# Optimization experiments

Measured on AMD Instinct MI355X. Metric: run time of the kernel, lower is better.

Reference implementation:

```python
import jax, jax.numpy as jnp
import numpy as np

B, SQ, SK, D, H, HD = 2, 2048, 2048, 1024, 16, 64


def setup_inputs() -> dict:
    key = jax.random.key(0)
    ks = jax.random.split(key, 10)
    s = 1.0 / np.sqrt(D)  # keep activations well-scaled
    return {
        "x": jax.random.normal(ks[0], (B, SQ, D), jnp.float32),
        "encoder_output": jax.random.normal(ks[1], (B, SK, D), jnp.float32),
        "Wq": jax.random.normal(ks[2], (H, D, HD), jnp.float32) * s,
        "bq": jax.random.normal(ks[3], (H, HD), jnp.float32) * 0.01,
        "Wk": jax.random.normal(ks[4], (H, D, HD), jnp.float32) * s,
        "bk": jax.random.normal(ks[5], (H, HD), jnp.float32) * 0.01,
        "Wv": jax.random.normal(ks[6], (H, D, HD), jnp.float32) * s,
        "bv": jax.random.normal(ks[7], (H, HD), jnp.float32) * 0.01,
        "Wo": jax.random.normal(ks[8], (D, D), jnp.float32) * s,
        "bo": jax.random.normal(ks[9], (D,), jnp.float32) * 0.01,
    }


def reference(x, encoder_output, Wq, bq, Wk, bk, Wv, bv, Wo, bo):
    # Batched per-head projections (equivalent to the per-head nn.Linear loop).
    q = jnp.einsum('bsd,hde->bhse', x, Wq) + bq[None, :, None, :]              # [B,H,SQ,HD]
    k = jnp.einsum('bsd,hde->bhse', encoder_output, Wk) + bk[None, :, None, :]  # [B,H,SK,HD]
    v = jnp.einsum('bsd,hde->bhse', encoder_output, Wv) + bv[None, :, None, :]  # [B,H,SK,HD]
    scale = 1.0 / jnp.sqrt(jnp.asarray(HD, q.dtype))
    scores = jnp.einsum('bhqe,bhke->bhqk', q, k) * scale                        # [B,H,SQ,SK]
    attn = jax.nn.softmax(scores, axis=-1)
    out = jnp.einsum('bhqk,bhke->bhqe', attn, v)                                # [B,H,SQ,HD]
    # concat heads along feature dim (head order matches torch.cat order)
    out = out.transpose(0, 2, 1, 3).reshape(out.shape[0], out.shape[2], -1)     # [B,SQ,D]
    # final linear; dropout is identity in eval mode
    return out @ Wo + bo
```

## Files before the change

kernel.cpp:

```cpp
#include <hip/hip_runtime.h>


typedef unsigned short u16;
typedef __bf16 bf16x8 __attribute__((ext_vector_type(8)));
typedef float f32x4 __attribute__((ext_vector_type(4)));
typedef float f32x16 __attribute__((ext_vector_type(16)));
typedef unsigned u32x2 __attribute__((ext_vector_type(2)));

#define B_ 2
#define SQ_ 2048
#define SK_ 2048
#define D_ 1024
#define H_ 16
#define HD_ 64

__device__ __forceinline__ u16 f2bf(float f) {
  union { float f; unsigned u; } c; c.f = f;
  unsigned u = c.u;
  return (u16)((u + 0x7fffu + ((u >> 16) & 1u)) >> 16);
}
__device__ __forceinline__ float bf2f(u16 h) {
  union { unsigned u; float f; } c; c.u = ((unsigned)h) << 16;
  return c.f;
}
__device__ __forceinline__ unsigned pack_bf16(float lo, float hi) {
  union { __bf16 h[2]; unsigned u; } c;
  c.h[0] = (__bf16)lo;
  c.h[1] = (__bf16)hi;
  return c.u;
}

#define GLOAD_LDS16(gp, lp)                                                  \
  __builtin_amdgcn_global_load_lds(                                          \
      (const __attribute__((address_space(1))) void*)(gp),                   \
      (__attribute__((address_space(3))) void*)(lp), 16, 0, 0)

__global__ __launch_bounds__(256) void prep_fused(const float* __restrict__ x,
                                                  const float* __restrict__ enc,
                                                  const float* __restrict__ Wq,
                                                  const float* __restrict__ Wk,
                                                  const float* __restrict__ Wv,
                                                  const float* __restrict__ Wo,
                                                  u16* __restrict__ xb,
                                                  u16* __restrict__ eb,
                                                  u16* __restrict__ WqT,
                                                  u16* __restrict__ WoT) {
  __shared__ float tile[64][65];
  const int id = blockIdx.x;
  const int tid = threadIdx.x;

  if (id < 8192) {
    const float* in = (id >= 4096) ? enc : x;
    u16* out = (id >= 4096) ? eb : xb;
    int i = (id & 4095) * 256 + tid;
    float4 v = ((const float4*)in)[i];
    uint2 p;
    p.x = (unsigned)f2bf(v.x) | ((unsigned)f2bf(v.y) << 16);
    p.y = (unsigned)f2bf(v.z) | ((unsigned)f2bf(v.w) << 16);
    ((uint2*)out)[i] = p;
    return;
  }

  if (id < 8960) {
    const int f = id - 8192;
    const int z48 = f >> 4, y = f & 15;
    const int mat = z48 >> 4, head = z48 & 15;
    const float* W = (mat == 0) ? Wq : (mat == 1 ? Wk : Wv);
    const float* ib = W + (long)head * 65536;
    u16* ob = WqT + ((long)mat << 20) + (long)head * 65536;
    const int r0 = y << 6;
#pragma unroll
    for (int i = 0; i < 16; ++i) {
      int idx = tid + (i << 8);
      int r = idx >> 6, c = idx & 63;
      tile[r][c] = ib[(long)(r0 + r) * 64 + c];
    }
    __syncthreads();
#pragma unroll
    for (int i = 0; i < 16; ++i) {
      int idx = tid + (i << 8);
      int cc = idx >> 6, rr = idx & 63;
      ob[(long)cc * 1024 + (r0 + rr)] = f2bf(tile[rr][cc]);
    }
    return;
  }

  {
    const int g = id - 8960;
    const int c0 = (g & 15) << 6, r0 = (g >> 4) << 6;
#pragma unroll
    for (int i = 0; i < 16; ++i) {
      int idx = tid + (i << 8);
      int r = idx >> 6, c = idx & 63;
      tile[r][c] = Wo[(long)(r0 + r) * 1024 + (c0 + c)];
    }
    __syncthreads();
#pragma unroll
    for (int i = 0; i < 16; ++i) {
      int idx = tid + (i << 8);
      int cc = idx >> 6, rr = idx & 63;
      WoT[(long)(c0 + cc) * 1024 + (r0 + rr)] = f2bf(tile[rr][cc]);
    }
  }
}

__global__ __launch_bounds__(256) void gemm_qkv(const u16* __restrict__ xb,
                                                const u16* __restrict__ eb,
                                                const u16* __restrict__ Wt3,
                                                const float* __restrict__ bq,
                                                const float* __restrict__ bk,
                                                const float* __restrict__ bv,
                                                u16* __restrict__ qws,
                                                u16* __restrict__ kws,
                                                u16* __restrict__ vT) {
  constexpr int M = 2048, N = 1024, K = 1024;
  __shared__ __align__(16) u16 As[128 * 64];
  __shared__ __align__(16) u16 Bs[128 * 64];
  const int tid = threadIdx.x;
  const int lane = tid & 63;
  const int wid = tid >> 6;
  const int l16 = lane & 15, quad = lane >> 4;
  const int wm = wid >> 1, wn = wid & 1;
  const int bn0g = blockIdx.x << 7;
  const int seg = bn0g >> 10;
  const int bn0 = bn0g & (N - 1);
  const int bm0 = blockIdx.y << 7;
  const u16* A = (seg == 0) ? xb : eb;
  const u16* Wt = Wt3 + ((long)seg << 20);
  const float* bias = (seg == 0) ? bq : (seg == 1 ? bk : bv);
  const long abase = (long)blockIdx.z * M * K;

  f32x4 acc[4][4];
#pragma unroll
  for (int i = 0; i < 4; ++i)
#pragma unroll
    for (int j = 0; j < 4; ++j) acc[i][j] = f32x4{0.f, 0.f, 0.f, 0.f};

  const int r0 = tid >> 3;
  const int c0s = ((tid & 7) ^ (r0 & 7)) << 3;
  const u16* agp = A + abase + (long)(bm0 + r0) * K + c0s;
  const u16* bgp = Wt + (long)(bn0 + r0) * K + c0s;
  u16* alp = As + tid * 8;
  u16* blp = Bs + tid * 8;

  for (int k0 = 0; k0 < K; k0 += 64) {
#pragma unroll
    for (int i = 0; i < 4; ++i) {
      GLOAD_LDS16(agp + k0 + (long)(32 * i) * K, alp + i * 2048);
      GLOAD_LDS16(bgp + k0 + (long)(32 * i) * K, blp + i * 2048);
    }
    __syncthreads();
#pragma unroll
    for (int kk = 0; kk < 2; ++kk) {
      const int csw = ((quad + 4 * kk) ^ (l16 & 7)) << 3;
      bf16x8 af[4], bfr[4];
#pragma unroll
      for (int mi = 0; mi < 4; ++mi)
        af[mi] = *(const bf16x8*)(As + (wm * 64 + mi * 16 + l16) * 64 + csw);
#pragma unroll
      for (int ni = 0; ni < 4; ++ni)
        bfr[ni] = *(const bf16x8*)(Bs + (wn * 64 + ni * 16 + l16) * 64 + csw);
#pragma unroll
      for (int mi = 0; mi < 4; ++mi)
#pragma unroll
        for (int ni = 0; ni < 4; ++ni)
          acc[mi][ni] = __builtin_amdgcn_mfma_f32_16x16x32_bf16(af[mi], bfr[ni],
                                                                acc[mi][ni], 0, 0, 0);
    }
    __syncthreads();
  }

  float bv4[4];
#pragma unroll
  for (int ni = 0; ni < 4; ++ni) bv4[ni] = bias[bn0 + wn * 64 + ni * 16 + l16];

  if (seg == 2) {
    const long zb = (long)blockIdx.z * N * M;
#pragma unroll
    for (int mi = 0; mi < 4; ++mi)
#pragma unroll
      for (int ni = 0; ni < 4; ++ni) {
        int colg = bn0 + wn * 64 + ni * 16 + l16;
        int rowg = bm0 + wm * 64 + mi * 16 + (quad << 2);
        ushort4 pk = make_ushort4(f2bf(acc[mi][ni][0] + bv4[ni]),
                                  f2bf(acc[mi][ni][1] + bv4[ni]),
                                  f2bf(acc[mi][ni][2] + bv4[ni]),
                                  f2bf(acc[mi][ni][3] + bv4[ni]));
        *(ushort4*)(vT + zb + (long)colg * M + rowg) = pk;
      }
  } else {
    u16* outp = seg ? kws : qws;
    const long cbase = (long)blockIdx.z * M * N;
#pragma unroll
    for (int mi = 0; mi < 4; ++mi)
#pragma unroll
      for (int ni = 0; ni < 4; ++ni)
#pragma unroll
        for (int r = 0; r < 4; ++r) {
          int row = bm0 + wm * 64 + mi * 16 + (quad << 2) + r;
          int col = bn0 + wn * 64 + ni * 16 + l16;
          outp[cbase + (long)row * N + col] = f2bf(acc[mi][ni][r] + bv4[ni]);
        }
  }
}

__global__ __launch_bounds__(256) void gemm_final(const u16* __restrict__ A,
                                                  const u16* __restrict__ Wt,
                                                  const float* __restrict__ bias,
                                                  float* __restrict__ C) {
  constexpr int M = 2048, N = 1024, K = 1024;
  __shared__ __align__(16) u16 As[64 * 64];
  __shared__ __align__(16) u16 Bs[128 * 64];
  const int tid = threadIdx.x;
  const int lane = tid & 63;
  const int wid = tid >> 6;
  const int l16 = lane & 15, quad = lane >> 4;
  const int bn0 = blockIdx.x << 7, bm0 = blockIdx.y << 6;

  f32x4 acc[4][2];
#pragma unroll
  for (int i = 0; i < 4; ++i)
#pragma unroll
    for (int j = 0; j < 2; ++j) acc[i][j] = f32x4{0.f, 0.f, 0.f, 0.f};

  const int r0 = tid >> 3;
  const int c0s = ((tid & 7) ^ (r0 & 7)) << 3;
  const long abase = (long)blockIdx.z * M * K;
  const u16* agp = A + abase + (long)(bm0 + r0) * K + c0s;
  const u16* bgp = Wt + (long)(bn0 + r0) * K + c0s;
  u16* alp = As + tid * 8;
  u16* blp = Bs + tid * 8;

  for (int k0 = 0; k0 < K; k0 += 64) {
#pragma unroll
    for (int i = 0; i < 2; ++i)
      GLOAD_LDS16(agp + k0 + (long)(32 * i) * K, alp + i * 2048);
#pragma unroll
    for (int i = 0; i < 4; ++i)
      GLOAD_LDS16(bgp + k0 + (long)(32 * i) * K, blp + i * 2048);
    __syncthreads();
#pragma unroll
    for (int kk = 0; kk < 2; ++kk) {
      const int csw = ((quad + 4 * kk) ^ (l16 & 7)) << 3;
      bf16x8 af[4], bfr[2];
#pragma unroll
      for (int mi = 0; mi < 4; ++mi)
        af[mi] = *(const bf16x8*)(As + (mi * 16 + l16) * 64 + csw);
#pragma unroll
      for (int ni = 0; ni < 2; ++ni)
        bfr[ni] = *(const bf16x8*)(Bs + (wid * 32 + ni * 16 + l16) * 64 + csw);
#pragma unroll
      for (int mi = 0; mi < 4; ++mi)
#pragma unroll
        for (int ni = 0; ni < 2; ++ni)
          acc[mi][ni] = __builtin_amdgcn_mfma_f32_16x16x32_bf16(af[mi], bfr[ni],
                                                                acc[mi][ni], 0, 0, 0);
    }
    __syncthreads();
  }

  float bv2[2];
#pragma unroll
  for (int ni = 0; ni < 2; ++ni) bv2[ni] = bias[bn0 + wid * 32 + ni * 16 + l16];
  const long cbase = (long)blockIdx.z * M * N;
#pragma unroll
  for (int mi = 0; mi < 4; ++mi)
#pragma unroll
    for (int ni = 0; ni < 2; ++ni)
#pragma unroll
      for (int r = 0; r < 4; ++r) {
        int row = bm0 + mi * 16 + (quad << 2) + r;
        int col = bn0 + wid * 32 + ni * 16 + l16;
        C[cbase + (long)row * N + col] = acc[mi][ni][r] + bv2[ni];
      }
}

#define ATTN_STAGE(kbase, vbase)                                              \
  do {                                                                        \
    GLOAD_LDS16(kp, (kbase) + st * 8);                                        \
    GLOAD_LDS16(kp + (long)32 * D_, (kbase) + 2048 + st * 8);                 \
    GLOAD_LDS16(vp, (vbase) + st * 8);                                        \
    GLOAD_LDS16(vp + (long)32 * SK_, (vbase) + 2048 + st * 8);                \
    kp += (long)64 * D_;                                                      \
    vp += 64;                                                                 \
  } while (0)

#define QK_BLOCK(Kb, sx0, sx1)                                                \
  do {                                                                        \
    {                                                                         \
      bf16x8 kf0 = *(const bf16x8*)((Kb) + ro0 + sw[0]);                      \
      bf16x8 kf1 = *(const bf16x8*)((Kb) + 2048 + ro0 + sw[0]);               \
      sx0 = __builtin_amdgcn_mfma_f32_32x32x16_bf16(kf0, qf[0], ZV, 0, 0, 0); \
      sx1 = __builtin_amdgcn_mfma_f32_32x32x16_bf16(kf1, qf[0], ZV, 0, 0, 0); \
    }                                                                         \
    _Pragma("unroll") for (int j = 1; j < 4; ++j) {                           \
      bf16x8 kf0 = *(const bf16x8*)((Kb) + ro0 + sw[j]);                      \
      bf16x8 kf1 = *(const bf16x8*)((Kb) + 2048 + ro0 + sw[j]);               \
      sx0 = __builtin_amdgcn_mfma_f32_32x32x16_bf16(kf0, qf[j], sx0, 0, 0, 0);\
      sx1 = __builtin_amdgcn_mfma_f32_32x32x16_bf16(kf1, qf[j], sx1, 0, 0, 0);\
    }                                                                         \
  } while (0)

#define EXPD(sx0, sx1)                                                        \
  do {                                                                        \
    _Pragma("unroll") for (int g = 0; g < 8; ++g) {                           \
      float a0 = __expf(sx0[2 * g]);                                          \
      float a1 = __expf(sx0[2 * g + 1]);                                      \
      float b0 = __expf(sx1[2 * g]);                                          \
      float b1 = __expf(sx1[2 * g + 1]);                                      \
      psA += a0 + a1;                                                         \
      psB += b0 + b1;                                                         \
      d0[g] = pack_bf16(a0, a1);                                              \
      d1[g] = pack_bf16(b0, b1);                                              \
    }                                                                         \
  } while (0)

#define PV_KS(Vb, dd, k1, ks)                                                 \
  do {                                                                        \
    u32x2 sA = __builtin_amdgcn_permlane32_swap(dd[4 * (k1)],                 \
                                                dd[4 * (k1) + 2], false,      \
                                                false);                       \
    u32x2 sB = __builtin_amdgcn_permlane32_swap(dd[4 * (k1) + 1],             \
                                                dd[4 * (k1) + 3], false,      \
                                                false);                       \
    union { unsigned u[4]; bf16x8 v; } pa;                                    \
    pa.u[0] = sA[0]; pa.u[1] = sB[0]; pa.u[2] = sA[1]; pa.u[3] = sB[1];       \
    bf16x8 v0 = *(const bf16x8*)((Vb) + ro0 + sw[ks]);                        \
    bf16x8 v1 = *(const bf16x8*)((Vb) + 2048 + ro0 + sw[ks]);                 \
    o0 = __builtin_amdgcn_mfma_f32_32x32x16_bf16(pa.v, v0, o0, 0, 0, 0);      \
    o1 = __builtin_amdgcn_mfma_f32_32x32x16_bf16(pa.v, v1, o1, 0, 0, 0);      \
  } while (0)

#define PV4(Vb)                                                               \
  do {                                                                        \
    PV_KS(Vb, d0, 0, 0);                                                      \
    PV_KS(Vb, d0, 1, 1);                                                      \
    PV_KS(Vb, d1, 0, 2);                                                      \
    PV_KS(Vb, d1, 1, 3);                                                      \
  } while (0)

__global__ __launch_bounds__(512) void attn_flash(const u16* __restrict__ q,
                                                  const u16* __restrict__ k,
                                                  const u16* __restrict__ vT,
                                                  u16* __restrict__ ctx) {
  __shared__ __align__(16) u16 SM[32768];

  const int tid = threadIdx.x;
  const int lane = tid & 63;
  const int wid = tid >> 6;
  const int half = wid >> 2;
  const int wq = wid & 3;
  const int l31 = lane & 31, h5 = lane >> 5;
  const int h = blockIdx.y, b = blockIdx.z;
  const int q0w = (blockIdx.x << 7) + (wq << 5);

  u16* Ksh = SM + half * 8192;
  u16* Vsh = SM + 16384 + half * 8192;

  bf16x8 qf[4];
  const u16* qp = q + ((long)(b * SQ_ + q0w + l31) * D_ + h * HD_ + 8 * h5);
#pragma unroll
  for (int j = 0; j < 4; ++j) {
    bf16x8 t = *(const bf16x8*)(qp + 16 * j);
#pragma unroll
    for (int e = 0; e < 8; ++e) t[e] = (__bf16)((float)t[e] * 0.125f);
    qf[j] = t;
  }

  const int st = tid & 255;
  const int srow = st >> 3;
  const int ssw = ((st & 7) ^ (srow & 7)) << 3;
  const u16* kp = k + ((long)(b * SK_ + (half << 10) + srow) * D_ + h * HD_ + ssw);
  const u16* vp = vT + ((long)(b * D_ + h * HD_ + srow) * SK_ + (half << 10) + ssw);

  const int ro0 = l31 << 6;
  int sw[4];
#pragma unroll
  for (int i = 0; i < 4; ++i) sw[i] = ((2 * i + h5) ^ (lane & 7)) << 3;

  f32x16 o0, o1, sA0, sA1;
  f32x16 ZV = {};
#pragma unroll
  for (int i = 0; i < 16; ++i) { o0[i] = 0.f; o1[i] = 0.f; }
  float psA = 0.f, psB = 0.f;
  unsigned d0[8], d1[8];

  ATTN_STAGE(Ksh, Vsh);

  for (int t = 0; t < 16; ++t) {
    const int cur = t & 1;
    __syncthreads();
    if (t < 15) ATTN_STAGE(Ksh + (cur ^ 1) * 4096, Vsh + (cur ^ 1) * 4096);
    QK_BLOCK(Ksh + cur * 4096, sA0, sA1);
    EXPD(sA0, sA1);
    PV4(Vsh + cur * 4096);
  }

  float ps = psA + psB;
  ps += __shfl_xor(ps, 32, 64);

  __syncthreads();
  float* cb = (float*)SM;
  const int wl = (wq << 6) | lane;
  if (half) {
#pragma unroll
    for (int r = 0; r < 16; ++r) {
      cb[r * 257 + wl] = o0[r];
      cb[(r + 16) * 257 + wl] = o1[r];
    }
    cb[8300 + wl] = ps;
  }
  __syncthreads();
  if (!half) {
#pragma unroll
    for (int r = 0; r < 16; ++r) {
      o0[r] += cb[r * 257 + wl];
      o1[r] += cb[(r + 16) * 257 + wl];
    }
    ps += cb[8300 + wl];
    float inv = 1.f / ps;
#pragma unroll
    for (int r = 0; r < 16; ++r) {
      const int crow = (r & 3) + 8 * (r >> 2) + 4 * h5;
      float dq = __shfl(inv, crow, 64);
      long base = (long)(b * SQ_ + q0w + crow) * D_ + h * HD_ + l31;
      ctx[base] = f2bf(o0[r] * dq);
      ctx[base + 32] = f2bf(o1[r] * dq);
    }
  }
}

extern "C" void kernel_launch(void* const* d_in, const int* in_sizes, int n_in,
                              void* d_out, int out_size, void* d_ws, size_t ws_size,
                              hipStream_t stream) {
  const float* x   = (const float*)d_in[0];
  const float* enc = (const float*)d_in[1];
  const float* Wq  = (const float*)d_in[2];
  const float* bq  = (const float*)d_in[3];
  const float* Wk  = (const float*)d_in[4];
  const float* bk  = (const float*)d_in[5];
  const float* Wv  = (const float*)d_in[6];
  const float* bv  = (const float*)d_in[7];
  const float* Wo  = (const float*)d_in[8];
  const float* bo  = (const float*)d_in[9];

  const long NE_X = (long)B_ * SQ_ * D_;
  const long NE_W = (long)D_ * D_;

  u16* outA = (u16*)d_out;
  u16* outB = outA + NE_X;
  u16* eb  = outB;
  u16* vTp = outA;

  u16* ws  = (u16*)d_ws;
  u16* WqT = ws;
  u16* WoT = WqT + 3 * NE_W;
  u16* qws = WoT + NE_W;
  u16* kws = qws + NE_X;
  u16* xb  = kws + NE_X;
  u16* ctx = xb;

  prep_fused<<<dim3(9216, 1, 1), 256, 0, stream>>>(x, enc, Wq, Wk, Wv, Wo,
                                                   xb, eb, WqT, WoT);

  gemm_qkv<<<dim3(24, 16, 2), 256, 0, stream>>>(xb, eb, WqT, bq, bk, bv,
                                                qws, kws, vTp);

  attn_flash<<<dim3(SQ_ / 128, H_, B_), 512, 0, stream>>>(qws, kws, vTp, ctx);

  gemm_final<<<dim3(8, 32, 2), 256, 0, stream>>>(ctx, WoT, bo, (float*)d_out);
}
```

Before: 210.3 us.

## Rewrite QKV GEMM with 256x256 tiles, double-buffered LDS and prioritized MFMA pipeline

The QKV projection GEMM moves from 128x128 tiles with 256 threads to 256x256 tiles with 512 threads (8 waves, each 128x64). It double-buffers the K slices in 128KB of LDS, issuing global-to-LDS loads for the next slice while the MFMAs for the current one run, with hand-placed barriers, waitcnts and setprio. This aims to hide global load latency and raise data reuse per tile. The cost is a grid of only 192 blocks with heavy LDS use (one block per CU), which may underfill the 256 CUs, plus fragile manual synchronization.

```diff
diff --git a/kernel.cpp b/kernel.cpp
--- a/kernel.cpp
+++ b/kernel.cpp
@@ -18,10 +18,6 @@
   union { float f; unsigned u; } c; c.f = f;
   unsigned u = c.u;
   return (u16)((u + 0x7fffu + ((u >> 16) & 1u)) >> 16);
-}
-__device__ __forceinline__ float bf2f(u16 h) {
-  union { unsigned u; float f; } c; c.u = ((unsigned)h) << 16;
-  return c.f;
 }
 __device__ __forceinline__ unsigned pack_bf16(float lo, float hi) {
   union { __bf16 h[2]; unsigned u; } c;
@@ -104,7 +100,55 @@
   }
 }
 
-__global__ __launch_bounds__(256) void gemm_qkv(const u16* __restrict__ xb,
+#define QBAR() asm volatile("s_barrier" ::: "memory")
+#define VMW4 asm volatile("s_waitcnt vmcnt(4)" ::: "memory")
+#define VMW0 asm volatile("s_waitcnt vmcnt(0)" ::: "memory")
+#define LGKM0 asm volatile("s_waitcnt lgkmcnt(0)" ::: "memory")
+#define PRIO1 __builtin_amdgcn_s_setprio(1)
+#define PRIO0 __builtin_amdgcn_s_setprio(0)
+
+#define ST_SLICE(gp, koff, dstu)                                              \
+  do {                                                                        \
+    GLOAD_LDS16((gp) + (koff), SMu + (dstu) + tid * 8);                       \
+    GLOAD_LDS16((gp) + (koff) + (long)128 * 1024, SMu + (dstu) + 4096 + tid * 8); \
+  } while (0)
+
+#define LDA4(dst, bufo, kko, mho)                                             \
+  _Pragma("unroll") for (int m2 = 0; m2 < 4; ++m2)                            \
+      dst[m2] = *(const bf16x8*)(SMu + (bufo) + (kko) + aob + (mho) + m2 * 512)
+
+#define LDB4(dst, bufo, kko)                                                  \
+  _Pragma("unroll") for (int n2 = 0; n2 < 4; ++n2)                            \
+      dst[n2] = *(const bf16x8*)(SMu + (bufo) + 16384 + (kko) + bob + n2 * 512)
+
+#define MM16(mh, av, bv_)                                                     \
+  _Pragma("unroll") for (int m2 = 0; m2 < 4; ++m2)                            \
+  _Pragma("unroll") for (int n2 = 0; n2 < 4; ++n2)                            \
+      acc[(mh) * 4 + m2][n2] = __builtin_amdgcn_mfma_f32_16x16x32_bf16(       \
+          av[m2], bv_[n2], acc[(mh) * 4 + m2][n2], 0, 0, 0)
+
+#define TILE_BODY(bo, so, kn)                                                 \
+  {                                                                           \
+    bf16x8 aF[4], aG[4], bF[4];                                               \
+                                      \
+    LDA4(aF, bo, 0, 0); LDB4(bF, bo, 0);                                      \
+    ST_SLICE(aS, (kn), (so) + 0);                                             \
+    QBAR(); LGKM0; PRIO1; MM16(0, aF, bF); PRIO0; QBAR();                     \
+                    \
+    LDA4(aG, bo, 0, 2048);                                                    \
+    ST_SLICE(bS, (kn), (so) + 16384);                                         \
+    QBAR(); LGKM0; PRIO1; MM16(1, aG, bF); PRIO0; VMW4; QBAR();               \
+                                      \
+    LDA4(aF, bo, 8192, 0); LDB4(bF, bo, 8192);                                \
+    ST_SLICE(aS, (kn) + 32, (so) + 8192);                                     \
+    QBAR(); LGKM0; PRIO1; MM16(0, aF, bF); PRIO0; QBAR();                     \
+                  \
+    LDA4(aG, bo, 8192, 2048);                                                 \
+    ST_SLICE(bS, (kn) + 32, (so) + 24576);                                    \
+    QBAR(); LGKM0; PRIO1; MM16(1, aG, bF); PRIO0; VMW4; QBAR();               \
+  }
+
+__global__ __launch_bounds__(512) void gemm_qkv(const u16* __restrict__ xb,
                                                 const u16* __restrict__ eb,
                                                 const u16* __restrict__ Wt3,
                                                 const float* __restrict__ bq,
@@ -114,60 +158,61 @@
                                                 u16* __restrict__ kws,
                                                 u16* __restrict__ vT) {
   constexpr int M = 2048, N = 1024, K = 1024;
-  __shared__ __align__(16) u16 As[128 * 64];
-  __shared__ __align__(16) u16 Bs[128 * 64];
+  __shared__ __align__(16) u16 SMu[65536];
+
   const int tid = threadIdx.x;
   const int lane = tid & 63;
   const int wid = tid >> 6;
+  const int wm = wid >> 2;
+  const int wn = wid & 3;
   const int l16 = lane & 15, quad = lane >> 4;
-  const int wm = wid >> 1, wn = wid & 1;
-  const int bn0g = blockIdx.x << 7;
+  const int qsw = (quad ^ ((l16 >> 1) & 3)) << 3;
+  const int aob = wm * 4096 + l16 * 32 + qsw;
+  const int bob = wn * 2048 + l16 * 32 + qsw;
+
+  const int bn0g = blockIdx.x << 8;
   const int seg = bn0g >> 10;
   const int bn0 = bn0g & (N - 1);
-  const int bm0 = blockIdx.y << 7;
+  const int bm0 = blockIdx.y << 8;
   const u16* A = (seg == 0) ? xb : eb;
   const u16* Wt = Wt3 + ((long)seg << 20);
   const float* bias = (seg == 0) ? bq : (seg == 1 ? bk : bv);
   const long abase = (long)blockIdx.z * M * K;
 
-  f32x4 acc[4][4];
-#pragma unroll
-  for (int i = 0; i < 4; ++i)
+  f32x4 acc[8][4];
+#pragma unroll
+  for (int i = 0; i < 8; ++i)
 #pragma unroll
     for (int j = 0; j < 4; ++j) acc[i][j] = f32x4{0.f, 0.f, 0.f, 0.f};
 
-  const int r0 = tid >> 3;
-  const int c0s = ((tid & 7) ^ (r0 & 7)) << 3;
-  const u16* agp = A + abase + (long)(bm0 + r0) * K + c0s;
-  const u16* bgp = Wt + (long)(bn0 + r0) * K + c0s;
-  u16* alp = As + tid * 8;
-  u16* blp = Bs + tid * 8;
-
-  for (int k0 = 0; k0 < K; k0 += 64) {
-#pragma unroll
-    for (int i = 0; i < 4; ++i) {
-      GLOAD_LDS16(agp + k0 + (long)(32 * i) * K, alp + i * 2048);
-      GLOAD_LDS16(bgp + k0 + (long)(32 * i) * K, blp + i * 2048);
-    }
-    __syncthreads();
-#pragma unroll
-    for (int kk = 0; kk < 2; ++kk) {
-      const int csw = ((quad + 4 * kk) ^ (l16 & 7)) << 3;
-      bf16x8 af[4], bfr[4];
-#pragma unroll
-      for (int mi = 0; mi < 4; ++mi)
-        af[mi] = *(const bf16x8*)(As + (wm * 64 + mi * 16 + l16) * 64 + csw);
-#pragma unroll
-      for (int ni = 0; ni < 4; ++ni)
-        bfr[ni] = *(const bf16x8*)(Bs + (wn * 64 + ni * 16 + l16) * 64 + csw);
-#pragma unroll
-      for (int mi = 0; mi < 4; ++mi)
-#pragma unroll
-        for (int ni = 0; ni < 4; ++ni)
-          acc[mi][ni] = __builtin_amdgcn_mfma_f32_16x16x32_bf16(af[mi], bfr[ni],
-                                                                acc[mi][ni], 0, 0, 0);
-    }
-    __syncthreads();
+  const int sr = tid >> 2;
+  const int sc2 = ((tid & 3) ^ ((sr >> 1) & 3)) << 3;
+  const u16* aS = A + abase + (long)(bm0 + sr) * K + sc2;
+  const u16* bS = Wt + (long)(bn0 + sr) * K + sc2;
+
+  ST_SLICE(aS, 0, 0);
+  ST_SLICE(bS, 0, 16384);
+  ST_SLICE(aS, 32, 8192);
+  ST_SLICE(bS, 32, 24576);
+  VMW4; QBAR();
+
+#pragma unroll 1
+  for (int tp = 0; tp < 7; ++tp) {
+    const int kb = tp * 128;
+    TILE_BODY(0, 32768, kb + 64);
+    TILE_BODY(32768, 0, kb + 128);
+  }
+  TILE_BODY(0, 32768, 960);
+  {
+    bf16x8 aF[4], aG[4], bF[4];
+    LDA4(aF, 32768, 0, 0); LDB4(bF, 32768, 0);
+    QBAR(); LGKM0; PRIO1; MM16(0, aF, bF); PRIO0; QBAR();
+    LDA4(aG, 32768, 0, 2048);
+    QBAR(); LGKM0; PRIO1; MM16(1, aG, bF); PRIO0; VMW0; QBAR();
+    LDA4(aF, 32768, 8192, 0); LDB4(bF, 32768, 8192);
+    QBAR(); LGKM0; PRIO1; MM16(0, aF, bF); PRIO0; QBAR();
+    LDA4(aG, 32768, 8192, 2048);
+    LGKM0; PRIO1; MM16(1, aG, bF); PRIO0;
   }
 
   float bv4[4];
@@ -177,11 +222,11 @@
   if (seg == 2) {
     const long zb = (long)blockIdx.z * N * M;
 #pragma unroll
-    for (int mi = 0; mi < 4; ++mi)
+    for (int mi = 0; mi < 8; ++mi)
 #pragma unroll
       for (int ni = 0; ni < 4; ++ni) {
         int colg = bn0 + wn * 64 + ni * 16 + l16;
-        int rowg = bm0 + wm * 64 + mi * 16 + (quad << 2);
+        int rowg = bm0 + wm * 128 + mi * 16 + (quad << 2);
         ushort4 pk = make_ushort4(f2bf(acc[mi][ni][0] + bv4[ni]),
                                   f2bf(acc[mi][ni][1] + bv4[ni]),
                                   f2bf(acc[mi][ni][2] + bv4[ni]),
@@ -192,12 +237,12 @@
     u16* outp = seg ? kws : qws;
     const long cbase = (long)blockIdx.z * M * N;
 #pragma unroll
-    for (int mi = 0; mi < 4; ++mi)
+    for (int mi = 0; mi < 8; ++mi)
 #pragma unroll
       for (int ni = 0; ni < 4; ++ni)
 #pragma unroll
         for (int r = 0; r < 4; ++r) {
-          int row = bm0 + wm * 64 + mi * 16 + (quad << 2) + r;
+          int row = bm0 + wm * 128 + mi * 16 + (quad << 2) + r;
           int col = bn0 + wn * 64 + ni * 16 + l16;
           outp[cbase + (long)row * N + col] = f2bf(acc[mi][ni][r] + bv4[ni]);
         }
@@ -463,8 +508,8 @@
   prep_fused<<<dim3(9216, 1, 1), 256, 0, stream>>>(x, enc, Wq, Wk, Wv, Wo,
                                                    xb, eb, WqT, WoT);
 
-  gemm_qkv<<<dim3(24, 16, 2), 256, 0, stream>>>(xb, eb, WqT, bq, bk, bv,
-                                                qws, kws, vTp);
+  gemm_qkv<<<dim3(12, 8, 2), 512, 0, stream>>>(xb, eb, WqT, bq, bk, bv,
+                                               qws, kws, vTp);
 
   attn_flash<<<dim3(SQ_ / 128, H_, B_), 512, 0, stream>>>(qws, kws, vTp, ctx);
 
```

New measurement: 205.3 us. 2.4% less time.
